# Kernel tuning notes

Hardware: AMD Instinct MI355X
Metric: run time of the kernel (lower is better)

Reference implementation:

```python
import jax, jax.numpy as jnp
import numpy as np

N = 200000   # nodes
E = 4000000  # edges
D = 32       # hidden dim (forced equal to edge-embed dim 32)
G = 512      # graphs in batch
OUT = 64     # conv5 output dim
BN_EPS = 1e-5


def _bn(h, g, b):
    # BatchNorm1d, training mode (fresh model): biased batch stats over node dim
    mu = jnp.mean(h, axis=0)
    var = jnp.var(h, axis=0)
    return g * (h - mu) * jax.lax.rsqrt(var + BN_EPS) + b


def _gine(h, src, dst, e, W1, b1, g, be, W2, b2, final_relu):
    # GINEConv (eps=0): out = MLP(x + sum_j ReLU(x_j + edge_attr))
    msg = jax.nn.relu(h[src] + e)                              # [E, D]
    agg = jax.ops.segment_sum(msg, dst, num_segments=h.shape[0])
    z = h + agg
    z = jax.nn.relu(_bn(z @ W1 + b1, g, be)) @ W2 + b2
    return jax.nn.relu(z) if final_relu else z


def setup_inputs() -> dict:
    key = jax.random.key(0)
    ks = jax.random.split(key, 16)
    xav = lambda k, shp: jax.random.uniform(k, shp, jnp.float32, -1.0, 1.0) * np.sqrt(6.0 / (shp[-2] + shp[-1]))
    x = jax.random.normal(ks[0], (N, D), jnp.float32)
    edge_index = jax.random.randint(ks[1], (2, E), 0, N, dtype=jnp.int32)
    edge_type = jax.random.randint(ks[2], (E,), 0, 2, dtype=jnp.int32)
    batch = jnp.sort(jax.random.randint(ks[3], (N,), 0, G, dtype=jnp.int32))
    emb = xav(ks[4], (2, D))  # xavier-initialized edge-type embedding
    # convs 1-4: Linear(D,D), BN(D), ReLU, Linear(D,D), ReLU  -> stacked [4,...]
    W1s = xav(ks[5], (4, D, D)); b1s = jnp.zeros((4, D))
    g1s = jnp.ones((4, D)); be1s = jnp.zeros((4, D))
    W2s = xav(ks[6], (4, D, D)); b2s = jnp.zeros((4, D))
    # conv 5: Linear(D,D), BN(D), ReLU, Linear(D,OUT)  (no final ReLU)
    w15 = xav(ks[7], (D, D)); b15 = jnp.zeros((D,))
    g5 = jnp.ones((D,)); be5 = jnp.zeros((D,))
    w25 = xav(ks[8], (D, OUT)); b25 = jnp.zeros((OUT,))
    return dict(x=x, edge_index=edge_index, edge_type=edge_type, batch=batch,
                emb=emb, W1s=W1s, b1s=b1s, g1s=g1s, be1s=be1s, W2s=W2s, b2s=b2s,
                w15=w15, b15=b15, g5=g5, be5=be5, w25=w25, b25=b25)


def reference(x, edge_index, edge_type, batch, emb, W1s, b1s, g1s, be1s, W2s, b2s,
              w15, b15, g5, be5, w25, b25):
    src, dst = edge_index[0], edge_index[1]
    e = emb[edge_type]                                          # [E, D]
    h = x
    for i in range(4):
        h = _gine(h, src, dst, e, W1s[i], b1s[i], g1s[i], be1s[i], W2s[i], b2s[i], True)
    h = _gine(h, src, dst, e, w15, b15, g5, be5, w25, b25, False)  # [N, OUT]
    mx = jax.ops.segment_max(h, batch, num_segments=G)
    cnt = jax.ops.segment_sum(jnp.ones((h.shape[0], 1), h.dtype), batch, num_segments=G)
    mn = jax.ops.segment_sum(h, batch, num_segments=G) / jnp.maximum(cnt, 1.0)
    return jnp.concatenate([mx, mn], axis=1)                    # [G, 2*OUT]
```

## Files before the change

### kernel.cpp

```cpp
#include <hip/hip_runtime.h>
#include <hip/hip_fp16.h>

#define NBLKA 2048

typedef _Float16 f16x2 __attribute__((ext_vector_type(2)));

__device__ __forceinline__ unsigned encf(float x) {
    unsigned u = __float_as_uint(x);
    return (u & 0x80000000u) ? ~u : (u | 0x80000000u);
}
__device__ __forceinline__ float decf(unsigned u) {
    u = (u & 0x80000000u) ? (u & 0x7FFFFFFFu) : ~u;
    return __uint_as_float(u);
}


__global__ __launch_bounds__(256) void passA_k(const int* __restrict__ dst, int E,
                                               int* __restrict__ cntMat, int bshift,
                                               int nblk, int nb2) {
    __shared__ int hist[512];
    hist[threadIdx.x] = 0; hist[threadIdx.x + 256] = 0;
    __syncthreads();
    int base = blockIdx.x * 4096;
#pragma unroll
    for (int r = 0; r < 16; r++) {
        int i = base + threadIdx.x + r * 256;
        if (i < E) atomicAdd(&hist[dst[i] >> bshift], 1);
    }
    __syncthreads();
    for (int bk = threadIdx.x; bk < nb2; bk += 256)
        cntMat[bk * nblk + blockIdx.x] = hist[bk];
}

__global__ void scanA_k(int* __restrict__ data, int total, int* __restrict__ chunkTot) {
    __shared__ int sd[256];
    int tid = threadIdx.x;
    int base = blockIdx.x * 2048 + tid * 8;
    int v[8]; int s = 0;
#pragma unroll
    for (int r = 0; r < 8; r++) {
        int idx = base + r;
        int x = (idx < total) ? data[idx] : 0;
        s += x; v[r] = s;
    }
    sd[tid] = s; __syncthreads();
    for (int off = 1; off < 256; off <<= 1) {
        int x = (tid >= off) ? sd[tid - off] : 0;
        __syncthreads();
        sd[tid] += x;
        __syncthreads();
    }
    int prev = (tid > 0) ? sd[tid - 1] : 0;
#pragma unroll
    for (int r = 0; r < 8; r++) {
        int idx = base + r;
        if (idx < total) data[idx] = v[r] + prev;
    }
    if (tid == 255) chunkTot[blockIdx.x] = sd[255];
}

__global__ void scanC3_k(int* __restrict__ data, int total,
                         const int* __restrict__ chunkTot, int nchunk) {
    __shared__ int sd[256];
    int tid = threadIdx.x;
    int v = (tid < nchunk) ? chunkTot[tid] : 0;
    sd[tid] = v; __syncthreads();
    for (int off = 1; off < 256; off <<= 1) {
        int x = (tid >= off) ? sd[tid - off] : 0;
        __syncthreads();
        sd[tid] += x;
        __syncthreads();
    }
    int boff = (blockIdx.x > 0) ? sd[blockIdx.x - 1] : 0;
    int base = blockIdx.x * 2048 + tid * 8;
#pragma unroll
    for (int r = 0; r < 8; r++) {
        int idx = base + r;
        if (idx < total) data[idx] += boff;
    }
}

__global__ __launch_bounds__(256) void passB_k(const int* __restrict__ ei,
                                               const int* __restrict__ ety, int E,
                                               const int* __restrict__ cntScan,
                                               unsigned* __restrict__ binned,
                                               int bshift, int sBits, int nblk, int nb2) {
    __shared__ unsigned stage[4096];
    __shared__ unsigned short bkid[4096];
    __shared__ int hist[512], sd[256], cursor[512], rebase[512];
    int tid = threadIdx.x;
    int base = blockIdx.x * 4096;
    hist[tid] = 0; hist[tid + 256] = 0;
    __syncthreads();

    unsigned ent[16];
    int bk[16];
    int lowmask = (1 << bshift) - 1;
    int dshift = sBits + 1;
#pragma unroll
    for (int r = 0; r < 16; r++) {
        int i = base + tid + r * 256;
        if (i < E) {
            int s = ei[i];
            int d = ei[E + i];
            int t = ety[i];
            ent[r] = ((unsigned)(d & lowmask) << dshift) | ((unsigned)t << sBits) | (unsigned)s;
            bk[r] = d >> bshift;
            atomicAdd(&hist[bk[r]], 1);
        } else bk[r] = -1;
    }
    __syncthreads();

    int v0 = hist[2 * tid], v1 = hist[2 * tid + 1];
    int sum2 = v0 + v1;
    sd[tid] = sum2; __syncthreads();
    for (int off = 1; off < 256; off <<= 1) {
        int x = (tid >= off) ? sd[tid - off] : 0;
        __syncthreads();
        sd[tid] += x;
        __syncthreads();
    }
    int exclPair = sd[tid] - sum2;
    __syncthreads();
    cursor[2 * tid] = exclPair;
    cursor[2 * tid + 1] = exclPair + v0;
    int b0 = 2 * tid, b1 = 2 * tid + 1;
    rebase[b0] = (b0 < nb2 && v0 > 0) ? (cntScan[b0 * nblk + blockIdx.x] - v0) - exclPair : 0;
    rebase[b1] = (b1 < nb2 && v1 > 0) ? (cntScan[b1 * nblk + blockIdx.x] - v1) - (exclPair + v0) : 0;
    __syncthreads();

#pragma unroll
    for (int r = 0; r < 16; r++) {
        if (bk[r] >= 0) {
            int p = atomicAdd(&cursor[bk[r]], 1);
            stage[p] = ent[r];
            bkid[p] = (unsigned short)bk[r];
        }
    }
    __syncthreads();

    int cnt = E - base; if (cnt > 4096) cnt = 4096;
    for (int i = tid; i < cnt; i += 256)
        binned[rebase[bkid[i]] + i] = stage[i];
}

__global__ __launch_bounds__(256) void passC_k(const unsigned* __restrict__ binned,
                                               const int* __restrict__ cntScan,
                                               int nblk, int* __restrict__ rowptr,
                                               unsigned* __restrict__ sorted,
                                               int N, int E, int bshift, int sBits,
                                               int nb2) {
    __shared__ int hist[512], cursor[512], sd[256];
    int tid = threadIdx.x;
    int b = blockIdx.x;
    int s = (b == 0) ? 0 : cntScan[b * nblk - 1];
    int e = cntScan[(b + 1) * nblk - 1];
    int nodeBase = b << bshift;
    int dshift = sBits + 1;

    hist[tid] = 0; hist[tid + 256] = 0;
    __syncthreads();
    for (int i = s + tid; i < e; i += 256)
        atomicAdd(&hist[(int)(binned[i] >> dshift)], 1);
    __syncthreads();

    int v0 = hist[2 * tid], v1 = hist[2 * tid + 1];
    int sum2 = v0 + v1;
    sd[tid] = sum2; __syncthreads();
    for (int off = 1; off < 256; off <<= 1) {
        int x = (tid >= off) ? sd[tid - off] : 0;
        __syncthreads();
        sd[tid] += x;
        __syncthreads();
    }
    int exclPair = sd[tid] - sum2;
    __syncthreads();
    cursor[2 * tid] = exclPair;
    cursor[2 * tid + 1] = exclPair + v0;
    int n0 = nodeBase + 2 * tid, n1 = nodeBase + 2 * tid + 1;
    if (n0 < N) rowptr[n0] = s + exclPair;
    if (n1 < N) rowptr[n1] = s + exclPair + v0;
    __syncthreads();

    for (int i = s + tid; i < e; i += 256) {
        unsigned en = binned[i];
        int ln = (int)(en >> dshift);
        int p = atomicAdd(&cursor[ln], 1);
        sorted[s + p] = en;
    }
    if (b == nb2 - 1 && tid == 0) rowptr[N] = E;
}

__global__ void prep_k(const float* __restrict__ x, unsigned* __restrict__ P,
                       unsigned* __restrict__ Q, int N,
                       unsigned* __restrict__ maxb, float* __restrict__ sumb, int G64) {
    int i = blockIdx.x * 256 + threadIdx.x;
    int tot = N * 16;
    if (i < tot) {
        float2 v = ((const float2*)x)[i];
        f16x2 hv;
        hv.x = (_Float16)v.x;
        hv.y = (_Float16)v.y;
        P[i] = *(unsigned*)&hv;
    }
    if (i < 16) {
        P[tot + i] = 0xFC00FC00u;
        Q[tot + i] = 0xFC00FC00u;
    }
    if (i < G64) { maxb[i] = 0x007FFFFFu; sumb[i] = 0.f; }
}

__global__ __launch_bounds__(256) void layerA_k(
    const unsigned* __restrict__ hin, const int* __restrict__ rowptr,
    const unsigned* __restrict__ sorted, const float* __restrict__ emb,
    const float* __restrict__ W1, const float* __restrict__ b1,
    float* __restrict__ tout, float* __restrict__ partial, int Nn, int sBits,
    unsigned sentw)
{
    float2* tout2 = (float2*)tout;
    int tid = threadIdx.x;
    int gl = tid & 31;
    int c = gl & 15;
    int slot = gl >> 4;
    int grp = tid >> 5;
    unsigned smask = (1u << sBits) - 1u;

    float2 w1c[16];
#pragma unroll
    for (int kk = 0; kk < 16; kk++)
        w1c[kk] = *(const float2*)&W1[(16 * slot + kk) * 32 + 2 * c];
    float2 b1p = *(const float2*)&b1[2 * c];
    f16x2 e0p, e1p, zero2;
    e0p.x = (_Float16)emb[2 * c];       e0p.y = (_Float16)emb[2 * c + 1];
    e1p.x = (_Float16)emb[32 + 2 * c];  e1p.y = (_Float16)emb[32 + 2 * c + 1];
    zero2.x = (_Float16)0.f;            zero2.y = (_Float16)0.f;

    __shared__ float zl[8][32];
    __shared__ float ls[8][32], lq[8][32];

    float2 bsum = {0.f, 0.f}, bsq = {0.f, 0.f};

    int gid0 = (blockIdx.x * 256 + tid) >> 5;
    int nG = (gridDim.x * 256) >> 5;

    for (int n = gid0; n < Nn; n += nG) {
        int es = rowptr[n], ee = rowptr[n + 1];
        float accx = 0.f, accy = 0.f;
        for (int e0 = es; e0 < ee; e0 += 32) {
            int idx = e0 + gl;
            unsigned pv = (idx < ee) ? sorted[idx] : sentw;
#pragma unroll
            for (int kk = 0; kk < 16; kk++) {
                unsigned p = (unsigned)__shfl((int)pv, kk, 16);
                unsigned s = p & smask;
                unsigned w = hin[s * 16u + (unsigned)c];
                f16x2 h2 = *reinterpret_cast<const f16x2*>(&w);
                f16x2 ev = (((p >> sBits) & 1u) != 0u) ? e1p : e0p;
                f16x2 rl = __builtin_elementwise_max(h2 + ev, zero2);
                accx += (float)rl.x;
                accy += (float)rl.y;
            }
        }
        accx += __shfl_xor(accx, 16);
        accy += __shfl_xor(accy, 16);
        unsigned wn = hin[(unsigned)n * 16u + (unsigned)c];
        f16x2 fn = *reinterpret_cast<const f16x2*>(&wn);
        accx += (float)fn.x;
        accy += (float)fn.y;

        if (slot == 0) { zl[grp][2 * c] = accx; zl[grp][2 * c + 1] = accy; }
        float tx = 0.f, ty = 0.f;
#pragma unroll
        for (int kk = 0; kk < 16; kk++) {
            float zk = zl[grp][16 * slot + kk];
            tx = fmaf(zk, w1c[kk].x, tx);
            ty = fmaf(zk, w1c[kk].y, ty);
        }
        tx += __shfl_xor(tx, 16);
        ty += __shfl_xor(ty, 16);
        tx += b1p.x; ty += b1p.y;
        if (slot == 0) { float2 tp; tp.x = tx; tp.y = ty; tout2[(unsigned)n * 16u + (unsigned)c] = tp; }
        bsum.x += tx; bsum.y += ty;
        bsq.x = fmaf(tx, tx, bsq.x);
        bsq.y = fmaf(ty, ty, bsq.y);
    }

    if (slot == 0) {
        ls[grp][2 * c] = bsum.x; ls[grp][2 * c + 1] = bsum.y;
        lq[grp][2 * c] = bsq.x;  lq[grp][2 * c + 1] = bsq.y;
    }
    __syncthreads();
    if (tid < 32) {
        float s = 0.f, q = 0.f;
#pragma unroll
        for (int r = 0; r < 8; r++) { s += ls[r][tid]; q += lq[r][tid]; }
        partial[blockIdx.x * 64 + tid] = s;
        partial[blockIdx.x * 64 + 32 + tid] = q;
    }
}

__global__ __launch_bounds__(256) void bnred1_k(const float* __restrict__ partial,
                                                float* __restrict__ partial2) {
    __shared__ float sd[4][64];
    int tid = threadIdx.x;
    int c = tid & 63, q = tid >> 6;
    int rowBase = blockIdx.x * 32 + q * 8;
    float s = 0.f;
#pragma unroll
    for (int r = 0; r < 8; r++) s += partial[(rowBase + r) * 64 + c];
    sd[q][c] = s;
    __syncthreads();
    if (q == 0) partial2[blockIdx.x * 64 + c] = sd[0][c] + sd[1][c] + sd[2][c] + sd[3][c];
}

__device__ __forceinline__ void bn_prologue(const float* __restrict__ partial2,
                                            const float* __restrict__ gamma,
                                            const float* __restrict__ beta,
                                            float invN, float* bnac ,
                                            float (*sd4)[64] ) {
    int tid = threadIdx.x;
    int c = tid & 63, q = tid >> 6;
    float s = 0.f;
#pragma unroll
    for (int r = 0; r < 16; r++) s += partial2[(q * 16 + r) * 64 + c];
    sd4[q][c] = s;
    __syncthreads();
    if (tid < 32) {
        float mu  = (sd4[0][tid] + sd4[1][tid] + sd4[2][tid] + sd4[3][tid]) * invN;
        float sq  = (sd4[0][tid + 32] + sd4[1][tid + 32] + sd4[2][tid + 32] + sd4[3][tid + 32]) * invN;
        float var = sq - mu * mu;
        float a = gamma[tid] * rsqrtf(var + 1e-5f);
        bnac[tid] = a;
        bnac[32 + tid] = beta[tid] - a * mu;
    }
    __syncthreads();
}

__global__ __launch_bounds__(256) void layerB32_k(
    const float* __restrict__ tin, const float* __restrict__ partial2,
    const float* __restrict__ gamma, const float* __restrict__ beta, float invN,
    const float* __restrict__ W2, const float* __restrict__ b2,
    unsigned* __restrict__ hout, int Nn)
{
    __shared__ float bnac[64];
    __shared__ float sd4[4][64];
    bn_prologue(partial2, gamma, beta, invN, bnac, sd4);

    int tid = threadIdx.x;
    int j = tid & 31, grp = tid >> 5;
    float a = bnac[j], c = bnac[32 + j];
    float wc[32];
#pragma unroll
    for (int k = 0; k < 32; k++) wc[k] = W2[k * 32 + j];
    float bj = b2[j];
    for (int n = blockIdx.x * 8 + grp; n < Nn; n += gridDim.x * 8) {
        float t = tin[n * 32 + j];
        float u = fmaxf(fmaf(a, t, c), 0.f);
        float o = bj;
#pragma unroll
        for (int k = 0; k < 32; k++) o = fmaf(__shfl(u, k, 32), wc[k], o);
        _Float16 hv = (_Float16)fmaxf(o, 0.f);
        unsigned hb = (unsigned)*reinterpret_cast<unsigned short*>(&hv);
        unsigned nb = (unsigned)__shfl_xor((int)hb, 1, 32);
        if ((j & 1) == 0) hout[(unsigned)n * 16u + (unsigned)(j >> 1)] = hb | (nb << 16);
    }
}

__global__ __launch_bounds__(256) void layerB64pool_k(
    const float* __restrict__ tin, const float* __restrict__ partial2,
    const float* __restrict__ gamma, const float* __restrict__ beta, float invN,
    const float* __restrict__ W2, const float* __restrict__ b2,
    const int* __restrict__ batch,
    unsigned* __restrict__ maxb, float* __restrict__ sumb, int Nn)
{
    __shared__ float bnac[64];
    __shared__ float sd4[4][64];
    bn_prologue(partial2, gamma, beta, invN, bnac, sd4);

    int tid = threadIdx.x;
    int j = tid & 31, grp = tid >> 5;
    float a = bnac[j], c = bnac[32 + j];
    float wlo[32], whi[32];
#pragma unroll
    for (int k = 0; k < 32; k++) { wlo[k] = W2[k * 64 + j]; whi[k] = W2[k * 64 + 32 + j]; }
    float blo = b2[j], bhi = b2[32 + j];

    int n0 = (blockIdx.x * 8 + grp) * 64;
    if (n0 >= Nn) return;
    int nend = n0 + 64; if (nend > Nn) nend = Nn;

    int curg = -1;
    float mxl = 0.f, mxh = 0.f, sml = 0.f, smh = 0.f;
    for (int n = n0; n < nend; n++) {
        float t = tin[n * 32 + j];
        float u = fmaxf(fmaf(a, t, c), 0.f);
        float olo = blo, ohi = bhi;
#pragma unroll
        for (int k = 0; k < 32; k++) {
            float uk = __shfl(u, k, 32);
            olo = fmaf(uk, wlo[k], olo);
            ohi = fmaf(uk, whi[k], ohi);
        }
        int gn = batch[n];
        if (gn != curg) {
            if (curg >= 0) {
                atomicMax(&maxb[curg * 64 + j], encf(mxl));
                atomicMax(&maxb[curg * 64 + 32 + j], encf(mxh));
                atomicAdd(&sumb[curg * 64 + j], sml);
                atomicAdd(&sumb[curg * 64 + 32 + j], smh);
            }
            curg = gn; mxl = olo; mxh = ohi; sml = olo; smh = ohi;
        } else {
            mxl = fmaxf(mxl, olo); mxh = fmaxf(mxh, ohi);
            sml += olo; smh += ohi;
        }
    }
    if (curg >= 0) {
        atomicMax(&maxb[curg * 64 + j], encf(mxl));
        atomicMax(&maxb[curg * 64 + 32 + j], encf(mxh));
        atomicAdd(&sumb[curg * 64 + j], sml);
        atomicAdd(&sumb[curg * 64 + 32 + j], smh);
    }
}

__global__ void final_k(const unsigned* __restrict__ maxb, const float* __restrict__ sumb,
                        const int* __restrict__ batch, int Nn, float* __restrict__ out)
{
    int g = blockIdx.x, tid = threadIdx.x;
    int a = 0, b = Nn;
    while (a < b) { int m = (a + b) >> 1; if (batch[m] < g) a = m + 1; else b = m; }
    int lo0 = a;
    a = 0; b = Nn;
    while (a < b) { int m = (a + b) >> 1; if (batch[m] < g + 1) a = m + 1; else b = m; }
    int hi0 = a;
    float inv = 1.f / fmaxf((float)(hi0 - lo0), 1.f);
    if (tid < 64) out[g * 128 + tid] = decf(maxb[g * 64 + tid]);
    else          out[g * 128 + tid] = sumb[g * 64 + (tid - 64)] * inv;
}

extern "C" void kernel_launch(void* const* d_in, const int* in_sizes, int n_in,
                              void* d_out, int out_size, void* d_ws, size_t ws_size,
                              hipStream_t stream) {
    const float* x    = (const float*)d_in[0];
    const int*   ei   = (const int*)d_in[1];
    const int*   ety  = (const int*)d_in[2];
    const int*   batch= (const int*)d_in[3];
    const float* emb  = (const float*)d_in[4];
    const float* W1s  = (const float*)d_in[5];
    const float* b1s  = (const float*)d_in[6];
    const float* g1s  = (const float*)d_in[7];
    const float* be1s = (const float*)d_in[8];
    const float* W2s  = (const float*)d_in[9];
    const float* b2s  = (const float*)d_in[10];
    const float* w15  = (const float*)d_in[11];
    const float* b15  = (const float*)d_in[12];
    const float* g5   = (const float*)d_in[13];
    const float* be5  = (const float*)d_in[14];
    const float* w25  = (const float*)d_in[15];
    const float* b25  = (const float*)d_in[16];

    int N = in_sizes[0] / 32;
    int E = in_sizes[1] / 2;
    int G = out_size / 128;

    int sBits = 1; while ((1 << sBits) < N + 1) sBits++;
    int bshift = 0; while (((N - 1) >> bshift) >= 512) bshift++;
    int nb2 = ((N - 1) >> bshift) + 1;
    int nblkE = (E + 4095) / 4096;

    char* wsb = (char*)d_ws;
    size_t o = 0;
    size_t hPkBytes = (size_t)(N + 1) * 16 * 4;
    size_t tbBytes = (size_t)N * 32 * 4;
    size_t binBytes = (size_t)E * 4;
    size_t rtb = tbBytes > binBytes ? tbBytes : binBytes;
    unsigned* P      = (unsigned*)(wsb + o); o += hPkBytes;
    unsigned* Q      = (unsigned*)(wsb + o); o += hPkBytes;
    float*    tb     = (float*)(wsb + o);
    unsigned* binned = (unsigned*)(wsb + o);
    o += rtb;
    int*      rowptr = (int*)(wsb + o);   o += ((size_t)N + 2) * 4;
    unsigned* sorted = (unsigned*)(wsb + o); o += (size_t)E * 4;
    int*      chunkTot = (int*)(wsb + o); o += 1024;
    float*    partial  = (float*)(wsb + o); o += (size_t)NBLKA * 64 * 4;
    float*    partial2 = (float*)(wsb + o); o += 64 * 64 * 4;
    unsigned* maxb     = (unsigned*)(wsb + o); o += (size_t)G * 64 * 4;
    float*    sumb     = (float*)(wsb + o); o += (size_t)G * 64 * 4;
    int*      cntMat   = (int*)(wsb + o); o += (size_t)nb2 * nblkE * 4;

    passA_k<<<nblkE, 256, 0, stream>>>(ei + E, E, cntMat, bshift, nblkE, nb2);
    int total2 = nb2 * nblkE;
    int nchunk2 = (total2 + 2047) / 2048;
    scanA_k<<<nchunk2, 256, 0, stream>>>(cntMat, total2, chunkTot);
    scanC3_k<<<nchunk2, 256, 0, stream>>>(cntMat, total2, chunkTot, nchunk2);
    passB_k<<<nblkE, 256, 0, stream>>>(ei, ety, E, cntMat, binned, bshift, sBits, nblkE, nb2);
    passC_k<<<nb2, 256, 0, stream>>>(binned, cntMat, nblkE, rowptr, sorted, N, E, bshift, sBits, nb2);
    prep_k<<<(N * 16 + 255) / 256, 256, 0, stream>>>(x, P, Q, N, maxb, sumb, G * 64);

    unsigned sentw = (unsigned)N;
    float invN = 1.f / (float)N;

    unsigned* inb = P;
    unsigned* outb = Q;
    for (int L = 0; L < 5; ++L) {
        const float* W1 = (L < 4) ? W1s + L * 1024 : w15;
        const float* b1 = (L < 4) ? b1s + L * 32  : b15;
        const float* ga = (L < 4) ? g1s + L * 32  : g5;
        const float* be = (L < 4) ? be1s + L * 32 : be5;
        const float* W2 = (L < 4) ? W2s + L * 1024 : w25;
        const float* b2 = (L < 4) ? b2s + L * 32  : b25;

        layerA_k<<<NBLKA, 256, 0, stream>>>(inb, rowptr, sorted, emb, W1, b1, tb, partial, N, sBits, sentw);
        bnred1_k<<<64, 256, 0, stream>>>(partial, partial2);
        if (L < 4) {
            layerB32_k<<<1024, 256, 0, stream>>>(tb, partial2, ga, be, invN, W2, b2, outb, N);
            unsigned* tmp = inb; inb = outb; outb = tmp;
        } else {
            layerB64pool_k<<<(N + 511) / 512, 256, 0, stream>>>(tb, partial2, ga, be, invN, W2, b2, batch, maxb, sumb, N);
        }
    }

    final_k<<<G, 128, 0, stream>>>(maxb, sumb, batch, N, (float*)d_out);
}
```

Measured before the change: 671.1 us.

## Store pre-BN intermediate as packed fp16 and restructure layerB32 matvec via LDS

The pre-BatchNorm activation buffer written by layerA and read by the layerB kernels now holds packed fp16 pairs instead of fp32, which halves that round-trip traffic. layerB32 also switches from 32 shuffles per node to the layerA pattern: each lane handles two columns, the input vector is staged in shared memory, and the two half-wave partial sums are combined with a single xor shuffle. The cost is some precision in the BN input, and BN statistics are still taken from the fp32 values.

```diff
diff --git a/kernel.cpp b/kernel.cpp
--- a/kernel.cpp
+++ b/kernel.cpp
@@ -12,6 +12,19 @@
 __device__ __forceinline__ float decf(unsigned u) {
     u = (u & 0x80000000u) ? (u & 0x7FFFFFFFu) : ~u;
     return __uint_as_float(u);
+}
+__device__ __forceinline__ unsigned packf16(float x, float y) {
+    f16x2 hv;
+    hv.x = (_Float16)x;
+    hv.y = (_Float16)y;
+    return *reinterpret_cast<unsigned*>(&hv);
+}
+__device__ __forceinline__ float2 unpackf16(unsigned w) {
+    f16x2 hv = *reinterpret_cast<const f16x2*>(&w);
+    float2 f;
+    f.x = (float)hv.x;
+    f.y = (float)hv.y;
+    return f;
 }
 
 
@@ -198,10 +211,7 @@
     int tot = N * 16;
     if (i < tot) {
         float2 v = ((const float2*)x)[i];
-        f16x2 hv;
-        hv.x = (_Float16)v.x;
-        hv.y = (_Float16)v.y;
-        P[i] = *(unsigned*)&hv;
+        P[i] = packf16(v.x, v.y);
     }
     if (i < 16) {
         P[tot + i] = 0xFC00FC00u;
@@ -214,10 +224,9 @@
     const unsigned* __restrict__ hin, const int* __restrict__ rowptr,
     const unsigned* __restrict__ sorted, const float* __restrict__ emb,
     const float* __restrict__ W1, const float* __restrict__ b1,
-    float* __restrict__ tout, float* __restrict__ partial, int Nn, int sBits,
+    unsigned* __restrict__ tout, float* __restrict__ partial, int Nn, int sBits,
     unsigned sentw)
 {
-    float2* tout2 = (float2*)tout;
     int tid = threadIdx.x;
     int gl = tid & 31;
     int c = gl & 15;
@@ -279,7 +288,7 @@
         tx += __shfl_xor(tx, 16);
         ty += __shfl_xor(ty, 16);
         tx += b1p.x; ty += b1p.y;
-        if (slot == 0) { float2 tp; tp.x = tx; tp.y = ty; tout2[(unsigned)n * 16u + (unsigned)c] = tp; }
+        if (slot == 0) tout[(unsigned)n * 16u + (unsigned)c] = packf16(tx, ty);
         bsum.x += tx; bsum.y += ty;
         bsq.x = fmaf(tx, tx, bsq.x);
         bsq.y = fmaf(ty, ty, bsq.y);
@@ -337,7 +346,7 @@
 }
 
 __global__ __launch_bounds__(256) void layerB32_k(
-    const float* __restrict__ tin, const float* __restrict__ partial2,
+    const unsigned* __restrict__ tin, const float* __restrict__ partial2,
     const float* __restrict__ gamma, const float* __restrict__ beta, float invN,
     const float* __restrict__ W2, const float* __restrict__ b2,
     unsigned* __restrict__ hout, int Nn)
@@ -347,27 +356,46 @@
     bn_prologue(partial2, gamma, beta, invN, bnac, sd4);
 
     int tid = threadIdx.x;
-    int j = tid & 31, grp = tid >> 5;
-    float a = bnac[j], c = bnac[32 + j];
-    float wc[32];
-#pragma unroll
-    for (int k = 0; k < 32; k++) wc[k] = W2[k * 32 + j];
-    float bj = b2[j];
-    for (int n = blockIdx.x * 8 + grp; n < Nn; n += gridDim.x * 8) {
-        float t = tin[n * 32 + j];
-        float u = fmaxf(fmaf(a, t, c), 0.f);
-        float o = bj;
-#pragma unroll
-        for (int k = 0; k < 32; k++) o = fmaf(__shfl(u, k, 32), wc[k], o);
-        _Float16 hv = (_Float16)fmaxf(o, 0.f);
-        unsigned hb = (unsigned)*reinterpret_cast<unsigned short*>(&hv);
-        unsigned nb = (unsigned)__shfl_xor((int)hb, 1, 32);
-        if ((j & 1) == 0) hout[(unsigned)n * 16u + (unsigned)(j >> 1)] = hb | (nb << 16);
+    int gl = tid & 31;
+    int c = gl & 15;
+    int slot = gl >> 4;
+    int grp = tid >> 5;
+
+    float2 w2c[16];
+#pragma unroll
+    for (int kk = 0; kk < 16; kk++)
+        w2c[kk] = *(const float2*)&W2[(16 * slot + kk) * 32 + 2 * c];
+    float2 a2 = *(const float2*)&bnac[2 * c];
+    float2 c2 = *(const float2*)&bnac[32 + 2 * c];
+    float2 b2p = *(const float2*)&b2[2 * c];
+
+    __shared__ float zl[8][32];
+
+    int gid0 = (blockIdx.x * 256 + tid) >> 5;
+    int nG = (gridDim.x * 256) >> 5;
+
+    for (int n = gid0; n < Nn; n += nG) {
+        float2 t2 = unpackf16(tin[(unsigned)n * 16u + (unsigned)c]);
+        float ux = fmaxf(fmaf(a2.x, t2.x, c2.x), 0.f);
+        float uy = fmaxf(fmaf(a2.y, t2.y, c2.y), 0.f);
+        if (slot == 0) { zl[grp][2 * c] = ux; zl[grp][2 * c + 1] = uy; }
+        float ox = 0.f, oy = 0.f;
+#pragma unroll
+        for (int kk = 0; kk < 16; kk++) {
+            float uk = zl[grp][16 * slot + kk];
+            ox = fmaf(uk, w2c[kk].x, ox);
+            oy = fmaf(uk, w2c[kk].y, oy);
+        }
+        ox += __shfl_xor(ox, 16);
+        oy += __shfl_xor(oy, 16);
+        ox = fmaxf(ox + b2p.x, 0.f);
+        oy = fmaxf(oy + b2p.y, 0.f);
+        if (slot == 0) hout[(unsigned)n * 16u + (unsigned)c] = packf16(ox, oy);
     }
 }
 
 __global__ __launch_bounds__(256) void layerB64pool_k(
-    const float* __restrict__ tin, const float* __restrict__ partial2,
+    const unsigned* __restrict__ tin, const float* __restrict__ partial2,
     const float* __restrict__ gamma, const float* __restrict__ beta, float invN,
     const float* __restrict__ W2, const float* __restrict__ b2,
     const int* __restrict__ batch,
@@ -392,7 +420,8 @@
     int curg = -1;
     float mxl = 0.f, mxh = 0.f, sml = 0.f, smh = 0.f;
     for (int n = n0; n < nend; n++) {
-        float t = tin[n * 32 + j];
+        float2 tp = unpackf16(tin[(unsigned)n * 16u + (unsigned)(j >> 1)]);
+        float t = (j & 1) ? tp.y : tp.x;
         float u = fmaxf(fmaf(a, t, c), 0.f);
         float olo = blo, ohi = bhi;
 #pragma unroll
@@ -471,12 +500,12 @@
     char* wsb = (char*)d_ws;
     size_t o = 0;
     size_t hPkBytes = (size_t)(N + 1) * 16 * 4;
-    size_t tbBytes = (size_t)N * 32 * 4;
+    size_t tbBytes = (size_t)N * 16 * 4;
     size_t binBytes = (size_t)E * 4;
     size_t rtb = tbBytes > binBytes ? tbBytes : binBytes;
     unsigned* P      = (unsigned*)(wsb + o); o += hPkBytes;
     unsigned* Q      = (unsigned*)(wsb + o); o += hPkBytes;
-    float*    tb     = (float*)(wsb + o);
+    unsigned* tb     = (unsigned*)(wsb + o);
     unsigned* binned = (unsigned*)(wsb + o);
     o += rtb;
     int*      rowptr = (int*)(wsb + o);   o += ((size_t)N + 2) * 4;
```

Result: faster. 576.6 us (-14.1%).
